# Kernel optimization log

Hardware: AMD Instinct MI355X
Metric: run time of the kernel (lower is better)

The kernel has to match this reference:

```python
import jax, jax.numpy as jnp
import numpy as np


def setup_inputs() -> dict:
    key = jax.random.key(0)
    ks = jax.random.split(key, 6)
    B, C, H, W, O = 8, 64, 64, 64, 64
    x = jax.random.normal(ks[0], (B, C, H, W), jnp.float32)
    wq = jax.random.normal(ks[1], (O, C), jnp.float32) * 0.1
    wk = jax.random.normal(ks[2], (O, C), jnp.float32) * 0.1
    wv = jax.random.normal(ks[3], (O, C), jnp.float32) * 0.1
    rel_w = jax.random.normal(ks[4], (O, W), jnp.float32)
    rel_h = jax.random.normal(ks[5], (O, H), jnp.float32)
    return {"x": x, "wq": wq, "wk": wk, "wv": wv,
            "rel_w": rel_w, "rel_h": rel_h,
            "kernel_size": 7, "padding": 3}


def reference(x, wq, wk, wv, rel_w, rel_h, kernel_size, padding):
    B, C, H, W = x.shape
    k, p = kernel_size, padding
    # 1x1 convs (no bias) == channel matmuls
    q = jnp.einsum('bchw,oc->bohw', x, wq)                      # [B,O,H,W]
    xp = jnp.pad(x, ((0, 0), (0, 0), (p, p), (p, p)))
    k_out = jnp.einsum('bchw,oc->bohw', xp, wk)                 # [B,O,H+2p,W+2p]
    v_out = jnp.einsum('bchw,oc->bohw', xp, wv)

    def patches(t):  # torch unfold(2).unfold(3) order: row offset slowest
        return jnp.stack([t[:, :, i:i + H, j:j + W]
                          for i in range(k) for j in range(k)], axis=-1)  # [B,O,H,W,k*k]

    kp = patches(k_out)
    vp = patches(v_out)
    # relative position logits (broadcast elementwise einsums)
    rel = q * rel_w[None, :, None, :] + q * rel_h[None, :, :, None]  # [B,O,H,W]
    logits = q[..., None] * kp + rel[..., None]                 # [B,O,H,W,k*k]
    attn = jax.nn.softmax(logits, axis=-1)
    return jnp.sum(attn * vp, axis=-1)                          # [B,O,H,W]
```

## Files before the change

### kernel.cpp

```cpp
#include <hip/hip_runtime.h>
#include <hip/hip_bf16.h>

#define HW 4096

__device__ float g_qkv[3 * 8 * 64 * HW];

__global__ __launch_bounds__(256) void qkv_proj(
    const float* __restrict__ x,
    const float* __restrict__ wq,
    const float* __restrict__ wk,
    const float* __restrict__ wv)
{
    __shared__ float xs[64][64];
    __shared__ float wl[3][64][64];

    const int t = threadIdx.x;
    const int b = blockIdx.x >> 6;
    const int h = blockIdx.x & 63;

    const float* mats[3] = { wq, wk, wv };
    for (int i = t; i < 3 * 4096; i += 256) {
        int m = i >> 12, r = i & 4095;
        (&wl[0][0][0])[i] = mats[m][r];
    }
    {
        const float* xrow = x + (size_t)b * 64 * HW + (size_t)h * 64;
        for (int i = t; i < 64 * 64; i += 256) {
            int c = i >> 6, w = i & 63;
            xs[c][w] = xrow[(size_t)c * HW + w];
        }
    }
    __syncthreads();

    const int w = t & 63;
    const int ou = t >> 6;
    float xr[64];
    #pragma unroll
    for (int c = 0; c < 64; ++c) xr[c] = xs[c][w];

    #pragma unroll
    for (int m = 0; m < 3; ++m) {
        float* op = g_qkv + ((size_t)m * 8 + b) * (64 * HW) + (size_t)h * 64 + w;
        #pragma unroll
        for (int oi = 0; oi < 16; ++oi) {
            const int o = oi * 4 + ou;
            float acc = 0.f;
            #pragma unroll
            for (int c = 0; c < 64; ++c)
                acc = fmaf(wl[m][o][c], xr[c], acc);
            op[(size_t)o * HW] = acc;
        }
    }
}

__global__ __launch_bounds__(256) void attn(float* __restrict__ out)
{
    __shared__ float kt[70][72];
    __shared__ float vt[70][72];
    const int t = threadIdx.x;
    const int b = blockIdx.x >> 6;
    const int o = blockIdx.x & 63;

    const float* qb = g_qkv + ((size_t)(0 * 8 + b) * 64 + o) * HW;
    const float* kb = g_qkv + ((size_t)(1 * 8 + b) * 64 + o) * HW;
    const float* vb = g_qkv + ((size_t)(2 * 8 + b) * 64 + o) * HW;

    for (int i = t; i < 70 * 70; i += 256) {
        int r = i / 70, c = i - r * 70;
        int gh = r - 3, gw = c - 3;
        float kk = 0.f, vv = 0.f;
        if ((unsigned)gh < 64u && (unsigned)gw < 64u) {
            kk = kb[gh * 64 + gw];
            vv = vb[gh * 64 + gw];
        }
        kt[r][c] = kk;
        vt[r][c] = vv;
    }
    __syncthreads();

    const int w = t & 63;
    #pragma unroll 1
    for (int pass = 0; pass < 4; ++pass) {
        const int hbase = (pass * 4 + (t >> 6)) * 4;
        float qv[4];
        float den[4] = {0.f, 0.f, 0.f, 0.f};
        float num[4] = {0.f, 0.f, 0.f, 0.f};
        #pragma unroll
        for (int q = 0; q < 4; ++q) qv[q] = qb[(hbase + q) * 64 + w];

        #pragma unroll
        for (int rr = 0; rr < 10; ++rr) {
            #pragma unroll
            for (int dj = 0; dj < 7; ++dj) {
                float kk = kt[hbase + rr][w + dj];
                float vv = vt[hbase + rr][w + dj];
                #pragma unroll
                for (int q = 0; q < 4; ++q) {
                    if (rr - q >= 0 && rr - q < 7) {
                        float l = fminf(fmaxf(qv[q] * kk, -60.f), 60.f);
                        float e = __expf(l);
                        den[q] += e;
                        num[q] = fmaf(e, vv, num[q]);
                    }
                }
            }
        }
        #pragma unroll
        for (int q = 0; q < 4; ++q)
            out[((size_t)(b * 64 + o)) * HW + (hbase + q) * 64 + w] = num[q] / den[q];
    }
}

extern "C" void kernel_launch(void* const* d_in, const int* in_sizes, int n_in,
                              void* d_out, int out_size, void* d_ws, size_t ws_size,
                              hipStream_t stream)
{
    qkv_proj<<<dim3(512), dim3(256), 0, stream>>>(
        (const float*)d_in[0], (const float*)d_in[1],
        (const float*)d_in[2], (const float*)d_in[3]);
    attn<<<dim3(512), dim3(256), 0, stream>>>((float*)d_out);
}
```

Measured before the change: 134.7 us.

## Read weights via scalar loads, interleave K/V in LDS, widen row blocking

The projection kernel stops staging the three weight matrices in shared memory. Because the output-row index is made wave-uniform, it reads weights straight from global memory as scalar loads. The attention kernel interleaves K and V in one shared array so a single float2 load fetches both, and each thread now handles 8 output rows per pass instead of 4. This reuses each loaded K/V row across more queries. It also removes the logit clamp before exp, which saves instructions but risks overflow if the logits are large.

```diff
diff --git a/kernel.cpp b/kernel.cpp
--- a/kernel.cpp
+++ b/kernel.cpp
@@ -12,42 +12,37 @@
     const float* __restrict__ wv)
 {
     __shared__ float xs[64][64];
-    __shared__ float wl[3][64][64];
-
     const int t = threadIdx.x;
     const int b = blockIdx.x >> 6;
     const int h = blockIdx.x & 63;
 
-    const float* mats[3] = { wq, wk, wv };
-    for (int i = t; i < 3 * 4096; i += 256) {
-        int m = i >> 12, r = i & 4095;
-        (&wl[0][0][0])[i] = mats[m][r];
-    }
-    {
-        const float* xrow = x + (size_t)b * 64 * HW + (size_t)h * 64;
-        for (int i = t; i < 64 * 64; i += 256) {
-            int c = i >> 6, w = i & 63;
-            xs[c][w] = xrow[(size_t)c * HW + w];
-        }
+    const float* xrow = x + (size_t)b * 64 * HW + (size_t)h * 64;
+    for (int i = t; i < 64 * 64; i += 256) {
+        int c = i >> 6, w = i & 63;
+        xs[c][w] = xrow[(size_t)c * HW + w];
     }
     __syncthreads();
 
     const int w = t & 63;
-    const int ou = t >> 6;
+    const int ou = __builtin_amdgcn_readfirstlane(t >> 6);
+
     float xr[64];
     #pragma unroll
     for (int c = 0; c < 64; ++c) xr[c] = xs[c][w];
 
+    const float* __restrict__ mats[3] = { wq, wk, wv };
     #pragma unroll
     for (int m = 0; m < 3; ++m) {
+        const float* __restrict__ wg = mats[m];
         float* op = g_qkv + ((size_t)m * 8 + b) * (64 * HW) + (size_t)h * 64 + w;
         #pragma unroll
         for (int oi = 0; oi < 16; ++oi) {
             const int o = oi * 4 + ou;
+            const float* __restrict__ wrow = wg + (o << 6);
             float acc = 0.f;
             #pragma unroll
             for (int c = 0; c < 64; ++c)
-                acc = fmaf(wl[m][o][c], xr[c], acc);
+                acc = fmaf(wrow[c], xr[c], acc);
             op[(size_t)o * HW] = acc;
         }
     }
@@ -55,8 +50,7 @@
 
 __global__ __launch_bounds__(256) void attn(float* __restrict__ out)
 {
-    __shared__ float kt[70][72];
-    __shared__ float vt[70][72];
+    __shared__ float kv[70][72][2];
     const int t = threadIdx.x;
     const int b = blockIdx.x >> 6;
     const int o = blockIdx.x & 63;
@@ -73,40 +67,39 @@
             kk = kb[gh * 64 + gw];
             vv = vb[gh * 64 + gw];
         }
-        kt[r][c] = kk;
-        vt[r][c] = vv;
+        kv[r][c][0] = kk;
+        kv[r][c][1] = vv;
     }
     __syncthreads();
 
     const int w = t & 63;
+    const int band = t >> 6;
     #pragma unroll 1
-    for (int pass = 0; pass < 4; ++pass) {
-        const int hbase = (pass * 4 + (t >> 6)) * 4;
-        float qv[4];
-        float den[4] = {0.f, 0.f, 0.f, 0.f};
-        float num[4] = {0.f, 0.f, 0.f, 0.f};
+    for (int pass = 0; pass < 2; ++pass) {
+        const int hbase = band * 16 + pass * 8;
+        float qv[8], den[8], num[8];
         #pragma unroll
-        for (int q = 0; q < 4; ++q) qv[q] = qb[(hbase + q) * 64 + w];
-
+        for (int q = 0; q < 8; ++q) {
+            qv[q] = qb[(hbase + q) * 64 + w];
+            den[q] = 0.f; num[q] = 0.f;
+        }
         #pragma unroll
-        for (int rr = 0; rr < 10; ++rr) {
+        for (int rr = 0; rr < 14; ++rr) {
             #pragma unroll
             for (int dj = 0; dj < 7; ++dj) {
-                float kk = kt[hbase + rr][w + dj];
-                float vv = vt[hbase + rr][w + dj];
+                const float2 kvp = *(const float2*)&kv[hbase + rr][w + dj][0];
                 #pragma unroll
-                for (int q = 0; q < 4; ++q) {
+                for (int q = 0; q < 8; ++q) {
                     if (rr - q >= 0 && rr - q < 7) {
-                        float l = fminf(fmaxf(qv[q] * kk, -60.f), 60.f);
-                        float e = __expf(l);
+                        float e = __expf(qv[q] * kvp.x);
                         den[q] += e;
-                        num[q] = fmaf(e, vv, num[q]);
+                        num[q] = fmaf(e, kvp.y, num[q]);
                     }
                 }
             }
         }
         #pragma unroll
-        for (int q = 0; q < 4; ++q)
+        for (int q = 0; q < 8; ++q)
             out[((size_t)(b * 64 + o)) * HW + (hbase + q) * 64 + w] = num[q] / den[q];
     }
 }
```

Result: slower. 145.7 us (+8.2%).
